# Optimization experiments

Hardware: AMD Instinct MI355X
Metric: run time of the kernel (lower is better)

## Reference

```python
import jax, jax.numpy as jnp
import numpy as np

B, N, DIM = 4, 2048, 1024
HEADS, DIM_HEAD = 16, 64
HIDDEN = HEADS * DIM_HEAD  # 1024
SCALE = 1.0 / np.sqrt(DIM_HEAD).astype(np.float32)


def setup_inputs() -> dict:
    key = jax.random.key(0)
    k1, k2, k3 = jax.random.split(key, 3)
    x = jax.random.normal(k1, (B, N, DIM), dtype=jnp.float32)
    # Linear(dim, 3*hidden, bias=False): stored as [in, out] for x @ W
    w_qkv = jax.random.normal(k2, (DIM, 3 * HIDDEN), dtype=jnp.float32) * (1.0 / np.sqrt(DIM))
    w_out = jax.random.normal(k3, (HIDDEN, DIM), dtype=jnp.float32) * (1.0 / np.sqrt(HIDDEN))
    b_out = jnp.zeros((DIM,), dtype=jnp.float32)
    return {"x": x, "w_qkv": w_qkv, "w_out": w_out, "b_out": b_out}


def reference(x, w_qkv, w_out, b_out):
    b, n, _ = x.shape
    qkv = x @ w_qkv                                  # [b, n, 3*hidden]
    q, k, v = jnp.split(qkv, 3, axis=-1)             # each [b, n, hidden]

    def to_heads(t):
        return t.reshape(b, n, HEADS, DIM_HEAD).transpose(0, 2, 1, 3)  # [b, h, n, d]

    q, k, v = to_heads(q), to_heads(k), to_heads(v)
    scores = jnp.einsum('bhid,bhjd->bhij', q, k) * SCALE   # [b, h, n_q, n_k]
    # Faithful to original: softmax over dim=2 (the QUERY axis), not keys.
    attn = jax.nn.softmax(scores, axis=2)
    y = jnp.einsum('bhij,bhjd->bhid', attn, v)             # [b, h, n, d]
    y = y.transpose(0, 2, 1, 3).reshape(b, n, HIDDEN)      # [b, n, hidden]
    return y @ w_out + b_out
```

## Files before the change

kernel.cpp:

```cpp
#include <hip/hip_runtime.h>
#include <math.h>
#include <stdint.h>

#define B_    4
#define N_    2048
#define DIM_  1024
#define H_    16
#define DH_   64
#define HID_  1024
#define RS_   3072
#define SCALE_ 0.125f
#define C2_   0.1803368801111204f

typedef unsigned short u16;
typedef unsigned int   u32;
typedef short  bf16x8 __attribute__((ext_vector_type(8)));
typedef u16    u16x8  __attribute__((ext_vector_type(8)));
typedef float  f32x4  __attribute__((ext_vector_type(4)));

__device__ inline u16 f2b(float x) {
    u32 u = __float_as_uint(x);
    return (u16)((u + 0x7fffu + ((u >> 16) & 1u)) >> 16);
}
__device__ inline float b2f(u16 x) {
    return __uint_as_float((u32)x << 16);
}

__device__ inline u32 pack2bf(float f0, float f1) {
    u32 u0 = __float_as_uint(f0) + 0x8000u;
    u32 u1 = __float_as_uint(f1) + 0x8000u;
    return __builtin_amdgcn_perm(u1, u0, 0x07060302u);
}

#if defined(__has_builtin)
#if __has_builtin(__builtin_amdgcn_global_load_lds)
#define USE_GLL 1
#endif
#endif

#ifdef USE_GLL
typedef const __attribute__((address_space(1))) u32* gas_ptr;
typedef __attribute__((address_space(3))) u32* las_ptr;
__device__ inline void gll16(const void* g, void* l) {
    __builtin_amdgcn_global_load_lds((gas_ptr)g, (las_ptr)l, 16, 0, 0);
}
#endif

__global__ __launch_bounds__(256) void cast_bf16(const float* __restrict__ in,
                                                 u16* __restrict__ out, int n) {
    int i = (blockIdx.x * 256 + threadIdx.x) * 8;
    if (i >= n) return;
    float4 a = *(const float4*)&in[i];
    float4 b = *(const float4*)&in[i + 4];
    u16x8 p;
    p[0] = f2b(a.x); p[1] = f2b(a.y); p[2] = f2b(a.z); p[3] = f2b(a.w);
    p[4] = f2b(b.x); p[5] = f2b(b.y); p[6] = f2b(b.z); p[7] = f2b(b.w);
    *(u16x8*)&out[i] = p;
}

__global__ __launch_bounds__(256) void transpose_cast(const float* __restrict__ W,
                                                      u16* __restrict__ Wt,
                                                      int K, int Nn) {
    __shared__ float t[64][65];
    const int tid = threadIdx.x;
    const int k0 = blockIdx.y * 64, n0 = blockIdx.x * 64;
    for (int idx = tid; idx < 64 * 16; idx += 256) {
        int r = idx >> 4, c4 = (idx & 15) * 4;
        float4 g = *(const float4*)&W[(size_t)(k0 + r) * Nn + n0 + c4];
        t[r][c4] = g.x; t[r][c4 + 1] = g.y; t[r][c4 + 2] = g.z; t[r][c4 + 3] = g.w;
    }
    __syncthreads();
    for (int idx = tid; idx < 64 * 8; idx += 256) {
        int n = idx >> 3, k8 = (idx & 7) * 8;
        u16x8 p;
        #pragma unroll
        for (int u = 0; u < 8; u++) p[u] = f2b(t[k8 + u][n]);
        *(u16x8*)&Wt[(size_t)(n0 + n) * K + k0 + k8] = p;
    }
}

__global__ __launch_bounds__(256) void build_vT(const u16* __restrict__ qkvb,
                                                const float* __restrict__ invl,
                                                u16* __restrict__ vT) {
    __shared__ u16 t[64 * 72];
    __shared__ float li[64];
    const int tid = threadIdx.x;
    const int bh = blockIdx.y, b = bh >> 4, h = bh & 15;
    const int j0 = blockIdx.x * 64;
    const u16* vbase = qkvb + (size_t)b * N_ * RS_ + 2 * HID_ + h * DH_;
    for (int idx = tid; idx < 512; idx += 256) {
        int r = idx >> 3, d8 = (idx & 7) * 8;
        *(u16x8*)&t[r * 72 + d8] = *(const u16x8*)&vbase[(size_t)(j0 + r) * RS_ + d8];
    }
    if (tid < 64) li[tid] = invl[(size_t)bh * N_ + j0 + tid];
    __syncthreads();
    {
        int d = tid >> 2, j16 = (tid & 3) * 16;
        u16x8 p0, p1;
        #pragma unroll
        for (int u = 0; u < 8; u++) {
            p0[u] = f2b(b2f(t[(j16 + u) * 72 + d]) * li[j16 + u]);
            p1[u] = f2b(b2f(t[(j16 + 8 + u) * 72 + d]) * li[j16 + 8 + u]);
        }
        size_t o = ((size_t)bh * DH_ + d) * N_ + j0 + j16;
        *(u16x8*)&vT[o] = p0;
        *(u16x8*)&vT[o + 8] = p1;
    }
}

template<int BF16OUT>
__global__ __launch_bounds__(256) void gemm_bt(const u16* __restrict__ A,
                                               const u16* __restrict__ Bt,
                                               const float* __restrict__ bias,
                                               void* __restrict__ Cout,
                                               int M, int Nn, int K) {
    __shared__ u16 at[128 * 32];
    __shared__ u16 bt[128 * 32];
    const int tid = threadIdx.x;
    const int lane = tid & 63, wave = tid >> 6;
    const int wr = wave >> 1, wc = wave & 1;
    const int mlane = lane & 15, quad = lane >> 4;
    const int m0 = blockIdx.y * 128, n0 = blockIdx.x * 128;
    const int r = tid >> 2, kc = (tid & 3) * 8;

    f32x4 acc[4][4] = {};

    for (int k0 = 0; k0 < K; k0 += 32) {
        __syncthreads();
#ifdef USE_GLL
        gll16(&A[(size_t)(m0 + r) * K + k0 + kc],       &at[r * 32 + kc]);
        gll16(&A[(size_t)(m0 + r + 64) * K + k0 + kc],  &at[(r + 64) * 32 + kc]);
        gll16(&Bt[(size_t)(n0 + r) * K + k0 + kc],      &bt[r * 32 + kc]);
        gll16(&Bt[(size_t)(n0 + r + 64) * K + k0 + kc], &bt[(r + 64) * 32 + kc]);
#else
        *(u16x8*)&at[r * 32 + kc]        = *(const u16x8*)&A[(size_t)(m0 + r) * K + k0 + kc];
        *(u16x8*)&at[(r + 64) * 32 + kc] = *(const u16x8*)&A[(size_t)(m0 + r + 64) * K + k0 + kc];
        *(u16x8*)&bt[r * 32 + kc]        = *(const u16x8*)&Bt[(size_t)(n0 + r) * K + k0 + kc];
        *(u16x8*)&bt[(r + 64) * 32 + kc] = *(const u16x8*)&Bt[(size_t)(n0 + r + 64) * K + k0 + kc];
#endif
        __syncthreads();

        bf16x8 af[4], bf[4];
        #pragma unroll
        for (int rt = 0; rt < 4; rt++)
            af[rt] = *(const bf16x8*)&at[(wr * 64 + rt * 16 + mlane) * 32 + quad * 8];
        #pragma unroll
        for (int ct = 0; ct < 4; ct++)
            bf[ct] = *(const bf16x8*)&bt[(wc * 64 + ct * 16 + mlane) * 32 + quad * 8];
        #pragma unroll
        for (int rt = 0; rt < 4; rt++)
            #pragma unroll
            for (int ct = 0; ct < 4; ct++)
                acc[rt][ct] = __builtin_amdgcn_mfma_f32_16x16x32_bf16(af[rt], bf[ct], acc[rt][ct], 0, 0, 0);
    }

    const int row0 = m0 + wr * 64 + quad * 4;
    const int col0 = n0 + wc * 64 + mlane;
    #pragma unroll
    for (int rt = 0; rt < 4; rt++)
        #pragma unroll
        for (int ct = 0; ct < 4; ct++) {
            int c = col0 + ct * 16;
            float bv = (!BF16OUT && bias != nullptr) ? bias[c] : 0.f;
            #pragma unroll
            for (int reg = 0; reg < 4; reg++) {
                int rr = row0 + rt * 16 + reg;
                float v = acc[rt][ct][reg] + bv;
                if (BF16OUT) ((u16*)Cout)[(size_t)rr * Nn + c] = f2b(v);
                else         ((float*)Cout)[(size_t)rr * Nn + c] = v;
            }
        }
}

__global__ __launch_bounds__(256) void attn_stats(const u16* __restrict__ qkvb,
                                                  float* __restrict__ invl) {
    __shared__ u16 kt[64 * 72];
    __shared__ u16 qt[4][64 * 72];
    __shared__ float red[4][64];

    const int tid = threadIdx.x;
    const int lane = tid & 63, wave = tid >> 6;
    const int mlane = lane & 15, quad = lane >> 4;
    const int bh = blockIdx.y, b = bh >> 4, h = bh & 15;
    const int j0 = blockIdx.x * 64;

    const u16* qbase = qkvb + (size_t)b * N_ * RS_ + h * DH_;
    const u16* kbase = qbase + HID_;

    for (int idx = tid; idx < 512; idx += 256) {
        int r = idx >> 3, d8 = (idx & 7) * 8;
        u16x8 raw = *(const u16x8*)&kbase[(size_t)(j0 + r) * RS_ + d8];
        u16x8 s;
        #pragma unroll
        for (int u = 0; u < 8; u++) s[u] = f2b(b2f((u16)raw[u]) * C2_);
        *(u16x8*)&kt[r * 72 + d8] = s;
    }
    __syncthreads();

    bf16x8 kf[4][2];
    #pragma unroll
    for (int t = 0; t < 4; t++)
        #pragma unroll
        for (int ks = 0; ks < 2; ks++)
            kf[t][ks] = *(const bf16x8*)&kt[(t * 16 + mlane) * 72 + ks * 32 + quad * 8];

    f32x4 acc[4] = {};
    u16* qw = &qt[wave][0];

    const int prr = lane >> 3, pd8 = (lane & 7) * 8;
    u16x8 pq[8];
    #pragma unroll
    for (int t = 0; t < 8; t++)
        pq[t] = *(const u16x8*)&qbase[(size_t)(wave * 64 + t * 8 + prr) * RS_ + pd8];

    for (int i0 = wave * 64; i0 < N_; i0 += 256) {
        #pragma unroll
        for (int t = 0; t < 8; t++)
            *(u16x8*)&qw[(t * 8 + prr) * 72 + pd8] = pq[t];
        int in = i0 + 256;
        if (in < N_) {
            #pragma unroll
            for (int t = 0; t < 8; t++)
                pq[t] = *(const u16x8*)&qbase[(size_t)(in + t * 8 + prr) * RS_ + pd8];
        }
        #pragma unroll
        for (int q4 = 0; q4 < 4; q4++) {
            bf16x8 bq0 = *(const bf16x8*)&qw[(q4 * 16 + mlane) * 72 + quad * 8];
            bf16x8 bq1 = *(const bf16x8*)&qw[(q4 * 16 + mlane) * 72 + 32 + quad * 8];
            #pragma unroll
            for (int t = 0; t < 4; t++) {
                f32x4 z = {0.f, 0.f, 0.f, 0.f};
                z = __builtin_amdgcn_mfma_f32_16x16x32_bf16(kf[t][0], bq0, z, 0, 0, 0);
                z = __builtin_amdgcn_mfma_f32_16x16x32_bf16(kf[t][1], bq1, z, 0, 0, 0);
                #pragma unroll
                for (int reg = 0; reg < 4; reg++)
                    acc[t][reg] += __builtin_amdgcn_exp2f(z[reg]);
            }
        }
    }

    #pragma unroll
    for (int t = 0; t < 4; t++)
        #pragma unroll
        for (int reg = 0; reg < 4; reg++) {
            float v = acc[t][reg];
            v += __shfl_xor(v, 1, 64);
            v += __shfl_xor(v, 2, 64);
            v += __shfl_xor(v, 4, 64);
            v += __shfl_xor(v, 8, 64);
            if (mlane == 0) red[wave][t * 16 + quad * 4 + reg] = v;
        }
    __syncthreads();
    if (tid < 64) {
        float l = red[0][tid] + red[1][tid] + red[2][tid] + red[3][tid];
        invl[(size_t)bh * N_ + j0 + tid] = 1.0f / l;
    }
}

__global__ __launch_bounds__(256) void attn_apply(const u16* __restrict__ qkvb,
                                                  const u16* __restrict__ vT,
                                                  u16* __restrict__ yb) {
    __shared__ u16 qp[128 * 72];
    __shared__ u16 kt[64 * 72];
    __shared__ u16 vt[64 * 72];

    const int tid = threadIdx.x;
    const int lane = tid & 63, wave = tid >> 6;
    const int mlane = lane & 15, quad = lane >> 4;
    const int bh = blockIdx.y, b = bh >> 4, h = bh & 15;
    const int i0 = blockIdx.x * 128;

    const u16* qbase = qkvb + (size_t)b * N_ * RS_ + h * DH_;
    const u16* kbase = qbase + HID_;
    const u16* vbase = vT + (size_t)bh * DH_ * N_;

    for (int idx = tid; idx < 1024; idx += 256) {
        int r = idx >> 3, d8 = (idx & 7) * 8;
        u16x8 raw = *(const u16x8*)&qbase[(size_t)(i0 + r) * RS_ + d8];
        u16x8 s;
        #pragma unroll
        for (int u = 0; u < 8; u++) s[u] = f2b(b2f((u16)raw[u]) * C2_);
        *(u16x8*)&qp[r * 72 + d8] = s;
    }
    __syncthreads();

    bf16x8 qf[2][2];
    #pragma unroll
    for (int rt = 0; rt < 2; rt++)
        #pragma unroll
        for (int ks = 0; ks < 2; ks++)
            qf[rt][ks] = *(const bf16x8*)&qp[(wave * 32 + rt * 16 + mlane) * 72 + ks * 32 + quad * 8];

    const int pr = tid >> 3, pc8 = (tid & 7) * 8;
    u16x8 pk0, pk1, pv0, pv1;
    pk0 = *(const u16x8*)&kbase[(size_t)pr * RS_ + pc8];
    pk1 = *(const u16x8*)&kbase[(size_t)(pr + 32) * RS_ + pc8];
    pv0 = *(const u16x8*)&vbase[(size_t)pr * N_ + pc8];
    pv1 = *(const u16x8*)&vbase[(size_t)(pr + 32) * N_ + pc8];

    f32x4 yacc[2][4] = {};

    for (int j0 = 0; j0 < N_; j0 += 64) {
        __syncthreads();
        *(u16x8*)&kt[pr * 72 + pc8]        = pk0;
        *(u16x8*)&kt[(pr + 32) * 72 + pc8] = pk1;
        *(u16x8*)&vt[pr * 72 + pc8]        = pv0;
        *(u16x8*)&vt[(pr + 32) * 72 + pc8] = pv1;
        __syncthreads();

        int jn = j0 + 64;
        if (jn < N_) {
            pk0 = *(const u16x8*)&kbase[(size_t)(jn + pr) * RS_ + pc8];
            pk1 = *(const u16x8*)&kbase[(size_t)(jn + pr + 32) * RS_ + pc8];
            pv0 = *(const u16x8*)&vbase[(size_t)pr * N_ + jn + pc8];
            pv1 = *(const u16x8*)&vbase[(size_t)(pr + 32) * N_ + jn + pc8];
        }

        f32x4 sc[2][4];
        #pragma unroll
        for (int k4 = 0; k4 < 4; k4++) {
            bf16x8 kf0 = *(const bf16x8*)&kt[(k4 * 16 + mlane) * 72 + quad * 8];
            bf16x8 kf1 = *(const bf16x8*)&kt[(k4 * 16 + mlane) * 72 + 32 + quad * 8];
            #pragma unroll
            for (int rt = 0; rt < 2; rt++) {
                f32x4 z = {0.f, 0.f, 0.f, 0.f};
                z = __builtin_amdgcn_mfma_f32_16x16x32_bf16(kf0, qf[rt][0], z, 0, 0, 0);
                z = __builtin_amdgcn_mfma_f32_16x16x32_bf16(kf1, qf[rt][1], z, 0, 0, 0);
                sc[rt][k4] = z;
            }
        }
        #pragma unroll
        for (int rt = 0; rt < 2; rt++)
            #pragma unroll
            for (int k4 = 0; k4 < 4; k4++) {
                float p0 = __builtin_amdgcn_exp2f(sc[rt][k4][0]);
                float p1 = __builtin_amdgcn_exp2f(sc[rt][k4][1]);
                float p2 = __builtin_amdgcn_exp2f(sc[rt][k4][2]);
                float p3 = __builtin_amdgcn_exp2f(sc[rt][k4][3]);
                uint2 w;
                w.x = pack2bf(p0, p1);
                w.y = pack2bf(p2, p3);
                *(uint2*)&qp[(wave * 32 + rt * 16 + mlane) * 72 + k4 * 16 + quad * 4] = w;
            }
        bf16x8 pf[2][2];
        #pragma unroll
        for (int rt = 0; rt < 2; rt++)
            #pragma unroll
            for (int ks = 0; ks < 2; ks++)
                pf[rt][ks] = *(const bf16x8*)&qp[(wave * 32 + rt * 16 + mlane) * 72 + ks * 32 + quad * 8];
        #pragma unroll
        for (int dt = 0; dt < 4; dt++) {
            bf16x8 vf0 = *(const bf16x8*)&vt[(dt * 16 + mlane) * 72 + quad * 8];
            bf16x8 vf1 = *(const bf16x8*)&vt[(dt * 16 + mlane) * 72 + 32 + quad * 8];
            #pragma unroll
            for (int rt = 0; rt < 2; rt++) {
                yacc[rt][dt] = __builtin_amdgcn_mfma_f32_16x16x32_bf16(pf[rt][0], vf0, yacc[rt][dt], 0, 0, 0);
                yacc[rt][dt] = __builtin_amdgcn_mfma_f32_16x16x32_bf16(pf[rt][1], vf1, yacc[rt][dt], 0, 0, 0);
            }
        }
    }

    #pragma unroll
    for (int rt = 0; rt < 2; rt++) {
        const size_t yrow0 = (size_t)b * N_ + i0 + wave * 32 + rt * 16 + quad * 4;
        #pragma unroll
        for (int dt = 0; dt < 4; dt++)
            #pragma unroll
            for (int reg = 0; reg < 4; reg++)
                yb[(yrow0 + reg) * HID_ + h * DH_ + dt * 16 + mlane] = f2b(yacc[rt][dt][reg]);
    }
}

extern "C" void kernel_launch(void* const* d_in, const int* in_sizes, int n_in,
                              void* d_out, int out_size, void* d_ws, size_t ws_size,
                              hipStream_t stream) {
    (void)in_sizes; (void)n_in; (void)out_size; (void)ws_size;

    const float* x     = (const float*)d_in[0];
    const float* w_qkv = (const float*)d_in[1];
    const float* w_out = (const float*)d_in[2];
    const float* b_out = (const float*)d_in[3];

    u16* xb    = (u16*)d_ws;
    u16* wqkvT = xb    + (size_t)8192 * 1024;
    u16* woutT = wqkvT + (size_t)3072 * 1024;
    u16* qkvb  = woutT + (size_t)1024 * 1024;
    u16* vTb   = qkvb  + (size_t)8192 * 3072;
    u16* yb    = vTb   + (size_t)64 * 64 * 2048;
    float* invl = (float*)(yb + (size_t)8192 * 1024);

    cast_bf16<<<4096, 256, 0, stream>>>(x, xb, 8192 * 1024);
    transpose_cast<<<dim3(3072 / 64, 1024 / 64), 256, 0, stream>>>(w_qkv, wqkvT, 1024, 3072);
    transpose_cast<<<dim3(1024 / 64, 1024 / 64), 256, 0, stream>>>(w_out, woutT, 1024, 1024);

    gemm_bt<1><<<dim3(3072 / 128, 8192 / 128), 256, 0, stream>>>(
        xb, wqkvT, nullptr, qkvb, 8192, 3072, 1024);

    attn_stats<<<dim3(N_ / 64, 64), 256, 0, stream>>>(qkvb, invl);
    build_vT<<<dim3(N_ / 64, 64), 256, 0, stream>>>(qkvb, invl, vTb);
    attn_apply<<<dim3(N_ / 128, 64), 256, 0, stream>>>(qkvb, vTb, yb);

    gemm_bt<0><<<dim3(1024 / 128, 8192 / 128), 256, 0, stream>>>(
        yb, woutT, b_out, d_out, 8192, 1024, 1024);
}
```

Before: 357.9 us.

## Switch attn_apply to 32x32 MFMA, keep P in registers, fold scale into Wq

```diff
diff --git a/kernel.cpp b/kernel.cpp
--- a/kernel.cpp
+++ b/kernel.cpp
@@ -9,7 +9,6 @@
 #define DH_   64
 #define HID_  1024
 #define RS_   3072
-#define SCALE_ 0.125f
 #define C2_   0.1803368801111204f
 
 typedef unsigned short u16;
@@ -17,6 +16,7 @@
 typedef short  bf16x8 __attribute__((ext_vector_type(8)));
 typedef u16    u16x8  __attribute__((ext_vector_type(8)));
 typedef float  f32x4  __attribute__((ext_vector_type(4)));
+typedef float  f32x16 __attribute__((ext_vector_type(16)));
 
 __device__ inline u16 f2b(float x) {
     u32 u = __float_as_uint(x);
@@ -60,7 +60,7 @@
 
 __global__ __launch_bounds__(256) void transpose_cast(const float* __restrict__ W,
                                                       u16* __restrict__ Wt,
-                                                      int K, int Nn) {
+                                                      int K, int Nn, int qcols) {
     __shared__ float t[64][65];
     const int tid = threadIdx.x;
     const int k0 = blockIdx.y * 64, n0 = blockIdx.x * 64;
@@ -72,9 +72,10 @@
     __syncthreads();
     for (int idx = tid; idx < 64 * 8; idx += 256) {
         int n = idx >> 3, k8 = (idx & 7) * 8;
+        float s = (n0 + n < qcols) ? C2_ : 1.0f;
         u16x8 p;
         #pragma unroll
-        for (int u = 0; u < 8; u++) p[u] = f2b(t[k8 + u][n]);
+        for (int u = 0; u < 8; u++) p[u] = f2b(t[k8 + u][n] * s);
         *(u16x8*)&Wt[(size_t)(n0 + n) * K + k0 + k8] = p;
     }
 }
@@ -189,11 +190,7 @@
 
     for (int idx = tid; idx < 512; idx += 256) {
         int r = idx >> 3, d8 = (idx & 7) * 8;
-        u16x8 raw = *(const u16x8*)&kbase[(size_t)(j0 + r) * RS_ + d8];
-        u16x8 s;
-        #pragma unroll
-        for (int u = 0; u < 8; u++) s[u] = f2b(b2f((u16)raw[u]) * C2_);
-        *(u16x8*)&kt[r * 72 + d8] = s;
+        *(u16x8*)&kt[r * 72 + d8] = *(const u16x8*)&kbase[(size_t)(j0 + r) * RS_ + d8];
     }
     __syncthreads();
 
@@ -260,36 +257,30 @@
 __global__ __launch_bounds__(256) void attn_apply(const u16* __restrict__ qkvb,
                                                   const u16* __restrict__ vT,
                                                   u16* __restrict__ yb) {
-    __shared__ u16 qp[128 * 72];
-    __shared__ u16 kt[64 * 72];
-    __shared__ u16 vt[64 * 72];
+    __shared__ u16 S[256 * 72];
 
     const int tid = threadIdx.x;
     const int lane = tid & 63, wave = tid >> 6;
-    const int mlane = lane & 15, quad = lane >> 4;
+    const int m31 = lane & 31, half = lane >> 5;
     const int bh = blockIdx.y, b = bh >> 4, h = bh & 15;
-    const int i0 = blockIdx.x * 128;
+    const int i0 = blockIdx.x * 256;
 
     const u16* qbase = qkvb + (size_t)b * N_ * RS_ + h * DH_;
     const u16* kbase = qbase + HID_;
     const u16* vbase = vT + (size_t)bh * DH_ * N_;
 
-    for (int idx = tid; idx < 1024; idx += 256) {
+    for (int idx = tid; idx < 2048; idx += 256) {
         int r = idx >> 3, d8 = (idx & 7) * 8;
-        u16x8 raw = *(const u16x8*)&qbase[(size_t)(i0 + r) * RS_ + d8];
-        u16x8 s;
-        #pragma unroll
-        for (int u = 0; u < 8; u++) s[u] = f2b(b2f((u16)raw[u]) * C2_);
-        *(u16x8*)&qp[r * 72 + d8] = s;
+        *(u16x8*)&S[r * 72 + d8] = *(const u16x8*)&qbase[(size_t)(i0 + r) * RS_ + d8];
     }
     __syncthreads();
 
-    bf16x8 qf[2][2];
-    #pragma unroll
-    for (int rt = 0; rt < 2; rt++)
-        #pragma unroll
-        for (int ks = 0; ks < 2; ks++)
-            qf[rt][ks] = *(const bf16x8*)&qp[(wave * 32 + rt * 16 + mlane) * 72 + ks * 32 + quad * 8];
+    bf16x8 qf[2][4];
+    #pragma unroll
+    for (int qc = 0; qc < 2; qc++)
+        #pragma unroll
+        for (int ks = 0; ks < 4; ks++)
+            qf[qc][ks] = *(const bf16x8*)&S[(wave * 64 + qc * 32 + m31) * 72 + ks * 16 + half * 8];
 
     const int pr = tid >> 3, pc8 = (tid & 7) * 8;
     u16x8 pk0, pk1, pv0, pv1;
@@ -298,14 +289,14 @@
     pv0 = *(const u16x8*)&vbase[(size_t)pr * N_ + pc8];
     pv1 = *(const u16x8*)&vbase[(size_t)(pr + 32) * N_ + pc8];
 
-    f32x4 yacc[2][4] = {};
+    f32x16 yacc[2][2] = {};
 
     for (int j0 = 0; j0 < N_; j0 += 64) {
         __syncthreads();
-        *(u16x8*)&kt[pr * 72 + pc8]        = pk0;
-        *(u16x8*)&kt[(pr + 32) * 72 + pc8] = pk1;
-        *(u16x8*)&vt[pr * 72 + pc8]        = pv0;
-        *(u16x8*)&vt[(pr + 32) * 72 + pc8] = pv1;
+        *(u16x8*)&S[pr * 72 + pc8]        = pk0;
+        *(u16x8*)&S[(pr + 32) * 72 + pc8] = pk1;
+        *(u16x8*)&S[(pr + 64) * 72 + pc8] = pv0;
+        *(u16x8*)&S[(pr + 96) * 72 + pc8] = pv1;
         __syncthreads();
 
         int jn = j0 + 64;
@@ -316,59 +307,72 @@
             pv1 = *(const u16x8*)&vbase[(size_t)(pr + 32) * N_ + jn + pc8];
         }
 
-        f32x4 sc[2][4];
-        #pragma unroll
-        for (int k4 = 0; k4 < 4; k4++) {
-            bf16x8 kf0 = *(const bf16x8*)&kt[(k4 * 16 + mlane) * 72 + quad * 8];
-            bf16x8 kf1 = *(const bf16x8*)&kt[(k4 * 16 + mlane) * 72 + 32 + quad * 8];
-            #pragma unroll
-            for (int rt = 0; rt < 2; rt++) {
-                f32x4 z = {0.f, 0.f, 0.f, 0.f};
-                z = __builtin_amdgcn_mfma_f32_16x16x32_bf16(kf0, qf[rt][0], z, 0, 0, 0);
-                z = __builtin_amdgcn_mfma_f32_16x16x32_bf16(kf1, qf[rt][1], z, 0, 0, 0);
-                sc[rt][k4] = z;
+        bf16x8 pa[2][4];
+        #pragma unroll
+        for (int kt = 0; kt < 2; kt++) {
+            bf16x8 ka[4];
+            #pragma unroll
+            for (int ks = 0; ks < 4; ks++)
+                ka[ks] = *(const bf16x8*)&S[(kt * 32 + m31) * 72 + ks * 16 + half * 8];
+
+            f32x16 sc[2] = {};
+            #pragma unroll
+            for (int ks = 0; ks < 4; ks++)
+                #pragma unroll
+                for (int qc = 0; qc < 2; qc++)
+                    sc[qc] = __builtin_amdgcn_mfma_f32_32x32x16_bf16(ka[ks], qf[qc][ks], sc[qc], 0, 0, 0);
+
+            #pragma unroll
+            for (int qc = 0; qc < 2; qc++) {
+                u32 U[4][2];
+                #pragma unroll
+                for (int rb = 0; rb < 4; rb++)
+                    #pragma unroll
+                    for (int pp = 0; pp < 2; pp++) {
+                        float e0 = __builtin_amdgcn_exp2f(sc[qc][4 * rb + 2 * pp]);
+                        float e1 = __builtin_amdgcn_exp2f(sc[qc][4 * rb + 2 * pp + 1]);
+                        U[rb][pp] = pack2bf(e0, e1);
+                    }
+                #pragma unroll
+                for (int ksl = 0; ksl < 2; ksl++) {
+                    const int rb0 = 2 * ksl;
+                    u32 a0 = U[rb0][0], a1 = U[rb0][1];
+                    u32 b0 = U[rb0 + 1][0], b1 = U[rb0 + 1][1];
+                    u32 e0 = half ? a0 : b0, e1 = half ? a1 : b1;
+                    u32 g0 = (u32)__shfl_xor((int)e0, 32, 64);
+                    u32 g1 = (u32)__shfl_xor((int)e1, 32, 64);
+                    u32 o0 = half ? b0 : a0, o1 = half ? b1 : a1;
+                    union { u32 u[4]; bf16x8 v; } cv;
+                    cv.u[0] = half ? g0 : o0;
+                    cv.u[1] = half ? g1 : o1;
+                    cv.u[2] = half ? o0 : g0;
+                    cv.u[3] = half ? o1 : g1;
+                    pa[qc][2 * kt + ksl] = cv.v;
+                }
             }
         }
-        #pragma unroll
-        for (int rt = 0; rt < 2; rt++)
-            #pragma unroll
-            for (int k4 = 0; k4 < 4; k4++) {
-                float p0 = __builtin_amdgcn_exp2f(sc[rt][k4][0]);
-                float p1 = __builtin_amdgcn_exp2f(sc[rt][k4][1]);
-                float p2 = __builtin_amdgcn_exp2f(sc[rt][k4][2]);
-                float p3 = __builtin_amdgcn_exp2f(sc[rt][k4][3]);
-                uint2 w;
-                w.x = pack2bf(p0, p1);
-                w.y = pack2bf(p2, p3);
-                *(uint2*)&qp[(wave * 32 + rt * 16 + mlane) * 72 + k4 * 16 + quad * 4] = w;
+
+        #pragma unroll
+        for (int ks16 = 0; ks16 < 4; ks16++) {
+            bf16x8 vb0 = *(const bf16x8*)&S[(64 + m31) * 72 + ks16 * 16 + half * 8];
+            bf16x8 vb1 = *(const bf16x8*)&S[(96 + m31) * 72 + ks16 * 16 + half * 8];
+            #pragma unroll
+            for (int qc = 0; qc < 2; qc++) {
+                yacc[qc][0] = __builtin_amdgcn_mfma_f32_32x32x16_bf16(pa[qc][ks16], vb0, yacc[qc][0], 0, 0, 0);
+                yacc[qc][1] = __builtin_amdgcn_mfma_f32_32x32x16_bf16(pa[qc][ks16], vb1, yacc[qc][1], 0, 0, 0);
             }
-        bf16x8 pf[2][2];
-        #pragma unroll
-        for (int rt = 0; rt < 2; rt++)
-            #pragma unroll
-            for (int ks = 0; ks < 2; ks++)
-                pf[rt][ks] = *(const bf16x8*)&qp[(wave * 32 + rt * 16 + mlane) * 72 + ks * 32 + quad * 8];
-        #pragma unroll
-        for (int dt = 0; dt < 4; dt++) {
-            bf16x8 vf0 = *(const bf16x8*)&vt[(dt * 16 + mlane) * 72 + quad * 8];
-            bf16x8 vf1 = *(const bf16x8*)&vt[(dt * 16 + mlane) * 72 + 32 + quad * 8];
-            #pragma unroll
-            for (int rt = 0; rt < 2; rt++) {
-                yacc[rt][dt] = __builtin_amdgcn_mfma_f32_16x16x32_bf16(pf[rt][0], vf0, yacc[rt][dt], 0, 0, 0);
-                yacc[rt][dt] = __builtin_amdgcn_mfma_f32_16x16x32_bf16(pf[rt][1], vf1, yacc[rt][dt], 0, 0, 0);
+        }
+    }
+
+    #pragma unroll
+    for (int qc = 0; qc < 2; qc++)
+        #pragma unroll
+        for (int dt = 0; dt < 2; dt++)
+            #pragma unroll
+            for (int reg = 0; reg < 16; reg++) {
+                int q = i0 + wave * 64 + qc * 32 + (reg & 3) + 8 * (reg >> 2) + 4 * half;
+                yb[((size_t)b * N_ + q) * HID_ + h * DH_ + dt * 32 + m31] = f2b(yacc[qc][dt][reg]);
             }
-        }
-    }
-
-    #pragma unroll
-    for (int rt = 0; rt < 2; rt++) {
-        const size_t yrow0 = (size_t)b * N_ + i0 + wave * 32 + rt * 16 + quad * 4;
-        #pragma unroll
-        for (int dt = 0; dt < 4; dt++)
-            #pragma unroll
-            for (int reg = 0; reg < 4; reg++)
-                yb[(yrow0 + reg) * HID_ + h * DH_ + dt * 16 + mlane] = f2b(yacc[rt][dt][reg]);
-    }
 }
 
 extern "C" void kernel_launch(void* const* d_in, const int* in_sizes, int n_in,
@@ -390,15 +394,15 @@
     float* invl = (float*)(yb + (size_t)8192 * 1024);
 
     cast_bf16<<<4096, 256, 0, stream>>>(x, xb, 8192 * 1024);
-    transpose_cast<<<dim3(3072 / 64, 1024 / 64), 256, 0, stream>>>(w_qkv, wqkvT, 1024, 3072);
-    transpose_cast<<<dim3(1024 / 64, 1024 / 64), 256, 0, stream>>>(w_out, woutT, 1024, 1024);
+    transpose_cast<<<dim3(3072 / 64, 1024 / 64), 256, 0, stream>>>(w_qkv, wqkvT, 1024, 3072, HID_);
+    transpose_cast<<<dim3(1024 / 64, 1024 / 64), 256, 0, stream>>>(w_out, woutT, 1024, 1024, 0);
 
     gemm_bt<1><<<dim3(3072 / 128, 8192 / 128), 256, 0, stream>>>(
         xb, wqkvT, nullptr, qkvb, 8192, 3072, 1024);
 
     attn_stats<<<dim3(N_ / 64, 64), 256, 0, stream>>>(qkvb, invl);
     build_vT<<<dim3(N_ / 64, 64), 256, 0, stream>>>(qkvb, invl, vTb);
-    attn_apply<<<dim3(N_ / 128, 64), 256, 0, stream>>>(qkvb, vTb, yb);
+    attn_apply<<<dim3(N_ / 256, 64), 256, 0, stream>>>(qkvb, vTb, yb);
 
     gemm_bt<0><<<dim3(1024 / 128, 8192 / 128), 256, 0, stream>>>(
         yb, woutT, b_out, d_out, 8192, 1024, 1024);
```

After: 357.6 us. No clear change (-0.1%).
